# Performance work log

Hardware: AMD Instinct MI355X
Metric: run time of the kernel (lower is better)

Reference implementation:

```python
import jax, jax.numpy as jnp
import numpy as np

HIDDEN_DIM = 1024
SEQ_LEN = 4096
D_IN = 1024


def setup_inputs() -> dict:
    key = jax.random.key(0)
    ks = jax.random.split(key, 9)
    s = 1.0 / np.sqrt(D_IN)
    return {
        "q": jax.random.normal(ks[0], (SEQ_LEN, D_IN), jnp.float32),
        "k": jax.random.normal(ks[1], (SEQ_LEN, D_IN), jnp.float32),
        "v": jax.random.normal(ks[2], (SEQ_LEN, D_IN), jnp.float32),
        "Wq": jax.random.normal(ks[3], (D_IN, HIDDEN_DIM), jnp.float32) * s,
        "bq": jnp.zeros((HIDDEN_DIM,), jnp.float32),
        "Wk": jax.random.normal(ks[4], (D_IN, HIDDEN_DIM), jnp.float32) * s,
        "bk": jnp.zeros((HIDDEN_DIM,), jnp.float32),
        "Wv": jax.random.normal(ks[5], (D_IN, HIDDEN_DIM), jnp.float32) * s,
        "bv": jnpp_zeros() if False else jnp.zeros((HIDDEN_DIM,), jnp.float32),
    }


def reference(q, k, v, Wq, bq, Wk, bk, Wv, bv):
    # Dense projections (flax Dense: x @ W + b)
    query = q @ Wq + bq          # [S, H]
    key_p = k @ Wk + bk          # [S, H]
    value = v @ Wv + bv          # [S, H]
    # scores = Q K^T / sqrt(hidden_dim)  -> [S, S]
    scores = jnp.matmul(query, key_p.T) / jnp.sqrt(jnp.float32(HIDDEN_DIM))
    weights = jax.nn.softmax(scores, axis=-1)
    context = jnp.matmul(weights, value)  # [S, H]
    return context
```

## Files before the change

### kernel.cpp

```cpp
#include <hip/hip_runtime.h>


typedef short short4v __attribute__((ext_vector_type(4)));
typedef short short8  __attribute__((ext_vector_type(8)));
typedef float f32x4   __attribute__((ext_vector_type(4)));

#define MFMA16 __builtin_amdgcn_mfma_f32_16x16x32_bf16

__device__ __forceinline__ short f2bf(float f) {
    union { float f; unsigned u; } x; x.f = f;
    unsigned r = (x.u + 0x7FFFu + ((x.u >> 16) & 1u)) >> 16;
    return (short)r;
}
__device__ __forceinline__ float bf2f(short s) {
    union { unsigned u; float f; } x;
    x.u = ((unsigned)(unsigned short)s) << 16; return x.f;
}
__device__ __forceinline__ void store_out(short* p, float v) { *p = f2bf(v); }
__device__ __forceinline__ void store_out(float* p, float v) { *p = v; }

__device__ __forceinline__ void gl2lds(const short* g, short* l) {
    __builtin_amdgcn_global_load_lds(
        (const __attribute__((address_space(1))) void*)g,
        (__attribute__((address_space(3))) void*)l, 16, 0, 0);
}

__global__ __launch_bounds__(256) void prep_w(
    const float* __restrict__ W0, const float* __restrict__ W1,
    const float* __restrict__ W2, short* __restrict__ Wt)
{
    __shared__ float tile[64][65];
    const float* W = blockIdx.z == 0 ? W0 : (blockIdx.z == 1 ? W1 : W2);
    short* T = Wt + (size_t)blockIdx.z * 1048576;
    const int c0 = blockIdx.x * 64;
    const int r0 = blockIdx.y * 64;
    const int tx = threadIdx.x & 63;
    const int ty = threadIdx.x >> 6;
    #pragma unroll
    for (int p = 0; p < 16; ++p) {
        int r = ty + p * 4;
        tile[r][tx] = W[(size_t)(r0 + r) * 1024 + c0 + tx];
    }
    __syncthreads();
    #pragma unroll
    for (int p = 0; p < 16; ++p) {
        int r = ty + p * 4;
        T[(size_t)(c0 + r) * 1024 + r0 + tx] = f2bf(tile[tx][r]);
    }
}

__global__ __launch_bounds__(256) void cast_qkv(
    const float* __restrict__ q, const float* __restrict__ k,
    const float* __restrict__ v, short* __restrict__ xb)
{
    const float* src = blockIdx.z == 0 ? q : (blockIdx.z == 1 ? k : v);
    short* dst = xb + (size_t)blockIdx.z * 4194304;
    for (int i = blockIdx.x * 256 + threadIdx.x; i < 1048576; i += 256 * 1024) {
        float4 f = ((const float4*)src)[i];
        short4v o;
        o[0] = f2bf(f.x); o[1] = f2bf(f.y); o[2] = f2bf(f.z); o[3] = f2bf(f.w);
        ((short4v*)dst)[i] = o;
    }
}

__global__ __launch_bounds__(256) void transpose_bf16(
    const short* __restrict__ in, short* __restrict__ out, int R, int C)
{
    __shared__ short tile[64][66];
    const int c0 = blockIdx.x * 64;
    const int r0 = blockIdx.y * 64;
    const int tx = threadIdx.x & 63;
    const int ty = threadIdx.x >> 6;
    #pragma unroll
    for (int p = 0; p < 16; ++p) {
        int r = ty + p * 4;
        tile[r][tx] = in[(size_t)(r0 + r) * C + c0 + tx];
    }
    __syncthreads();
    #pragma unroll
    for (int p = 0; p < 16; ++p) {
        int r = ty + p * 4;
        out[(size_t)(c0 + r) * R + r0 + tx] = tile[tx][r];
    }
}

template <typename TOut, int MODE>
__global__ __launch_bounds__(256) void gemm_lds(
    const short* __restrict__ A, const short* __restrict__ Bt,
    const float* __restrict__ b0, const float* __restrict__ b1,
    const float* __restrict__ b2, TOut* __restrict__ C,
    int M, int N, int Kd, int lda, int ldb, float scale, int kiters)
{
    __shared__ short As[128 * 32];
    __shared__ short Bs[128 * 32];

    const int t    = threadIdx.x;
    const int lane = t & 63;
    const int wv   = t >> 6;
    const int n0 = blockIdx.x * 128;
    const int m0 = blockIdx.y * 128;

    const float* bias = nullptr;
    int kbeg = 0;
    if constexpr (MODE == 1) {
        const int z = blockIdx.z;
        A  += (size_t)z * M * lda;
        Bt += (size_t)z * N * ldb;
        C  += (size_t)z * M * N;
        bias = z == 0 ? b0 : (z == 1 ? b1 : b2);
    }
    if constexpr (MODE == 2) {
        kbeg = blockIdx.z * kiters * 32;
        C += (size_t)blockIdx.z * M * N;
    }
    (void)b0; (void)b1; (void)b2;

    const int srow = wv * 32 + (lane >> 2);
    const int cl   = ((lane & 3) ^ ((lane >> 4) & 3)) * 8;
    const short* pA0 = A  + (size_t)(m0 + srow) * lda + kbeg + cl;
    const short* pA1 = pA0 + (size_t)16 * lda;
    const short* pB0 = Bt + (size_t)(n0 + srow) * ldb + kbeg + cl;
    const short* pB1 = pB0 + (size_t)16 * ldb;
    short* lA0 = &As[(wv * 2 + 0) * 512];
    short* lA1 = &As[(wv * 2 + 1) * 512];
    short* lB0 = &Bs[(wv * 2 + 0) * 512];
    short* lB1 = &Bs[(wv * 2 + 1) * 512];

    const int wm = wv & 1, wn = wv >> 1;
    const int lr = lane & 15, lq = lane >> 4;
    const int swz = ((lq ^ ((lr >> 2) & 3))) * 8;

    f32x4 acc[4][4];
    #pragma unroll
    for (int i = 0; i < 4; ++i)
        #pragma unroll
        for (int j = 0; j < 4; ++j) {
            f32x4 z = {0.f, 0.f, 0.f, 0.f};
            acc[i][j] = z;
        }

    for (int kk = 0; kk < kiters; ++kk) {
        gl2lds(pA0, lA0); gl2lds(pA1, lA1);
        gl2lds(pB0, lB0); gl2lds(pB1, lB1);
        pA0 += 32; pA1 += 32; pB0 += 32; pB1 += 32;
        __syncthreads();

        short8 af[4], bfr[4];
        #pragma unroll
        for (int i = 0; i < 4; ++i)
            af[i] = *(const short8*)&As[(wm * 64 + i * 16 + lr) * 32 + swz];
        #pragma unroll
        for (int j = 0; j < 4; ++j)
            bfr[j] = *(const short8*)&Bs[(wn * 64 + j * 16 + lr) * 32 + swz];
        #pragma unroll
        for (int i = 0; i < 4; ++i)
            #pragma unroll
            for (int j = 0; j < 4; ++j)
                acc[i][j] = MFMA16(af[i], bfr[j], acc[i][j], 0, 0, 0);
        __syncthreads();
    }

    #pragma unroll
    for (int i = 0; i < 4; ++i) {
        #pragma unroll
        for (int j = 0; j < 4; ++j) {
            const int crow = m0 + wm * 64 + i * 16 + lq * 4;
            const int ccol = n0 + wn * 64 + j * 16 + lr;
            float bb = 0.f;
            if constexpr (MODE == 1) bb = bias[ccol];
            #pragma unroll
            for (int r = 0; r < 4; ++r) {
                float val = acc[i][j][r] * scale + bb;
                store_out(&C[(size_t)(crow + r) * N + ccol], val);
            }
        }
    }
}

__global__ __launch_bounds__(256) void softmax_bf16(short* __restrict__ S)
{
    const int row = blockIdx.x;
    short8* r8 = (short8*)(S + (size_t)row * 4096);
    const int t = threadIdx.x;

    float x[16];
    #pragma unroll
    for (int i = 0; i < 2; ++i) {
        short8 raw = r8[t + 256 * i];
        #pragma unroll
        for (int j = 0; j < 8; ++j) x[8 * i + j] = bf2f(raw[j]);
    }
    float m = -1e30f;
    #pragma unroll
    for (int i = 0; i < 16; ++i) m = fmaxf(m, x[i]);
    #pragma unroll
    for (int off = 32; off > 0; off >>= 1) m = fmaxf(m, __shfl_xor(m, off));

    __shared__ float redm[4], reds[4];
    const int wv = t >> 6;
    if ((t & 63) == 0) redm[wv] = m;
    __syncthreads();
    m = fmaxf(fmaxf(redm[0], redm[1]), fmaxf(redm[2], redm[3]));

    float s = 0.f;
    #pragma unroll
    for (int i = 0; i < 16; ++i) { x[i] = __expf(x[i] - m); s += x[i]; }
    #pragma unroll
    for (int off = 32; off > 0; off >>= 1) s += __shfl_xor(s, off);
    if ((t & 63) == 0) reds[wv] = s;
    __syncthreads();
    s = reds[0] + reds[1] + reds[2] + reds[3];
    const float inv = 1.f / s;

    #pragma unroll
    for (int i = 0; i < 2; ++i) {
        short8 o;
        #pragma unroll
        for (int j = 0; j < 8; ++j) o[j] = f2bf(x[8 * i + j] * inv);
        r8[t + 256 * i] = o;
    }
}

__global__ __launch_bounds__(256) void combine(
    const float* __restrict__ p0, const float* __restrict__ p1,
    float* __restrict__ out)
{
    for (int i = blockIdx.x * 256 + threadIdx.x; i < 1048576; i += 256 * 1024) {
        float4 a = ((const float4*)p0)[i];
        float4 b = ((const float4*)p1)[i];
        float4 o; o.x = a.x + b.x; o.y = a.y + b.y;
        o.z = a.z + b.z; o.w = a.w + b.w;
        ((float4*)out)[i] = o;
    }
}

extern "C" void kernel_launch(void* const* d_in, const int* in_sizes, int n_in,
                              void* d_out, int out_size, void* d_ws, size_t ws_size,
                              hipStream_t stream)
{
    const float* q  = (const float*)d_in[0];
    const float* k  = (const float*)d_in[1];
    const float* v  = (const float*)d_in[2];
    const float* Wq = (const float*)d_in[3];
    const float* bq = (const float*)d_in[4];
    const float* Wk = (const float*)d_in[5];
    const float* bk = (const float*)d_in[6];
    const float* Wv = (const float*)d_in[7];
    const float* bv = (const float*)d_in[8];
    float* out = (float*)d_out;

    char* ws = (char*)d_ws;
    const size_t MB = 1ull << 20;
    short* Wt = (short*)(ws + 0);
    short* xb = (short*)(ws + 6 * MB);
    short* pr = (short*)(ws + 30 * MB);
    short* Vt = (short*)(ws + 54 * MB);
    short* S  = (short*)(ws + 62 * MB);
    float* p0 = (float*)(ws + 0);
    float* p1 = p0 + 4194304;

    prep_w<<<dim3(16, 16, 3), 256, 0, stream>>>(Wq, Wk, Wv, Wt);
    cast_qkv<<<dim3(1024, 1, 3), 256, 0, stream>>>(q, k, v, xb);
    gemm_lds<short, 1><<<dim3(8, 32, 3), 256, 0, stream>>>(
        xb, Wt, bq, bk, bv, pr, 4096, 1024, 1024, 1024, 1024, 1.f, 32);
    transpose_bf16<<<dim3(16, 64), 256, 0, stream>>>(pr + 2 * 4194304, Vt, 4096, 1024);
    gemm_lds<short, 0><<<dim3(32, 32), 256, 0, stream>>>(
        pr, pr + 4194304, nullptr, nullptr, nullptr, S,
        4096, 4096, 1024, 1024, 1024, 0.03125f, 32);
    softmax_bf16<<<4096, 256, 0, stream>>>(S);
    gemm_lds<float, 2><<<dim3(8, 32, 2), 256, 0, stream>>>(
        S, Vt, nullptr, nullptr, nullptr, p0,
        4096, 1024, 4096, 4096, 4096, 1.f, 64);
    combine<<<1024, 256, 0, stream>>>(p0, p1, out);
}
```

Measured before the change: 293.3 us.

## Deepen GEMM K-tile to 64, add grouped rasterization, fuse V transpose into projection

The GEMM kernel now stages 64-wide K slices with an XOR swizzle, which halves the number of loop iterations and barriers. Blocks are remapped into groups of 8 row-tiles to improve L2 reuse. The V projection blocks write a transposed output through LDS, so the separate transpose kernel is removed and Vt reuses the freed workspace region. The cost is doubled LDS per block, which may reduce occupancy.

```diff
diff --git a/kernel.cpp b/kernel.cpp
--- a/kernel.cpp
+++ b/kernel.cpp
@@ -63,42 +63,29 @@
     }
 }
 
-__global__ __launch_bounds__(256) void transpose_bf16(
-    const short* __restrict__ in, short* __restrict__ out, int R, int C)
-{
-    __shared__ short tile[64][66];
-    const int c0 = blockIdx.x * 64;
-    const int r0 = blockIdx.y * 64;
-    const int tx = threadIdx.x & 63;
-    const int ty = threadIdx.x >> 6;
-    #pragma unroll
-    for (int p = 0; p < 16; ++p) {
-        int r = ty + p * 4;
-        tile[r][tx] = in[(size_t)(r0 + r) * C + c0 + tx];
-    }
-    __syncthreads();
-    #pragma unroll
-    for (int p = 0; p < 16; ++p) {
-        int r = ty + p * 4;
-        out[(size_t)(c0 + r) * R + r0 + tx] = tile[tx][r];
-    }
-}
-
 template <typename TOut, int MODE>
-__global__ __launch_bounds__(256) void gemm_lds(
+__global__ __launch_bounds__(256) void gemm64(
     const short* __restrict__ A, const short* __restrict__ Bt,
     const float* __restrict__ b0, const float* __restrict__ b1,
     const float* __restrict__ b2, TOut* __restrict__ C,
+    short* __restrict__ Vt,
     int M, int N, int Kd, int lda, int ldb, float scale, int kiters)
 {
-    __shared__ short As[128 * 32];
-    __shared__ short Bs[128 * 32];
+    constexpr int LDSN = (MODE == 1) ? (128 * 136) : (128 * 64 * 2);
+    __shared__ short Lds[LDSN];
+    short* As = Lds;
+    short* Bs = Lds + 128 * 64;
 
     const int t    = threadIdx.x;
     const int lane = t & 63;
     const int wv   = t >> 6;
-    const int n0 = blockIdx.x * 128;
-    const int m0 = blockIdx.y * 128;
+
+    const int nb  = gridDim.x;
+    const int bid = blockIdx.y * nb + blockIdx.x;
+    const int band   = bid / (8 * nb);
+    const int within = bid - band * 8 * nb;
+    const int m0 = (band * 8 + (within & 7)) * 128;
+    const int n0 = (within >> 3) * 128;
 
     const float* bias = nullptr;
     int kbeg = 0;
@@ -110,25 +97,23 @@
         bias = z == 0 ? b0 : (z == 1 ? b1 : b2);
     }
     if constexpr (MODE == 2) {
-        kbeg = blockIdx.z * kiters * 32;
+        kbeg = blockIdx.z * kiters * 64;
         C += (size_t)blockIdx.z * M * N;
     }
     (void)b0; (void)b1; (void)b2;
 
-    const int srow = wv * 32 + (lane >> 2);
-    const int cl   = ((lane & 3) ^ ((lane >> 4) & 3)) * 8;
-    const short* pA0 = A  + (size_t)(m0 + srow) * lda + kbeg + cl;
-    const short* pA1 = pA0 + (size_t)16 * lda;
-    const short* pB0 = Bt + (size_t)(n0 + srow) * ldb + kbeg + cl;
-    const short* pB1 = pB0 + (size_t)16 * ldb;
-    short* lA0 = &As[(wv * 2 + 0) * 512];
-    short* lA1 = &As[(wv * 2 + 1) * 512];
-    short* lB0 = &Bs[(wv * 2 + 0) * 512];
-    short* lB1 = &Bs[(wv * 2 + 1) * 512];
+    const int sr = lane >> 3;
+    const int sc = (lane & 7) ^ sr;
+    const short* pA = A  + (size_t)(m0 + wv * 32 + sr) * lda + kbeg + sc * 8;
+    const short* pB = Bt + (size_t)(n0 + wv * 32 + sr) * ldb + kbeg + sc * 8;
+    const size_t a8 = (size_t)8 * lda;
+    const size_t b8 = (size_t)8 * ldb;
+    short* lA = As + wv * 2048;
+    short* lB = Bs + wv * 2048;
 
     const int wm = wv & 1, wn = wv >> 1;
     const int lr = lane & 15, lq = lane >> 4;
-    const int swz = ((lq ^ ((lr >> 2) & 3))) * 8;
+    const int xkey = lr & 7;
 
     f32x4 acc[4][4];
     #pragma unroll
@@ -140,26 +125,58 @@
         }
 
     for (int kk = 0; kk < kiters; ++kk) {
-        gl2lds(pA0, lA0); gl2lds(pA1, lA1);
-        gl2lds(pB0, lB0); gl2lds(pB1, lB1);
-        pA0 += 32; pA1 += 32; pB0 += 32; pB1 += 32;
+        #pragma unroll
+        for (int r = 0; r < 4; ++r) gl2lds(pA + r * a8, lA + r * 512);
+        #pragma unroll
+        for (int r = 0; r < 4; ++r) gl2lds(pB + r * b8, lB + r * 512);
+        pA += 64; pB += 64;
         __syncthreads();
 
-        short8 af[4], bfr[4];
-        #pragma unroll
-        for (int i = 0; i < 4; ++i)
-            af[i] = *(const short8*)&As[(wm * 64 + i * 16 + lr) * 32 + swz];
-        #pragma unroll
-        for (int j = 0; j < 4; ++j)
-            bfr[j] = *(const short8*)&Bs[(wn * 64 + j * 16 + lr) * 32 + swz];
-        #pragma unroll
-        for (int i = 0; i < 4; ++i)
+        #pragma unroll
+        for (int h = 0; h < 2; ++h) {
+            short8 af[4], bfr[4];
+            #pragma unroll
+            for (int i = 0; i < 4; ++i)
+                af[i] = *(const short8*)
+                    &As[(wm * 64 + i * 16 + lr) * 64 + (((h * 4 + lq) ^ xkey) * 8)];
             #pragma unroll
             for (int j = 0; j < 4; ++j)
-                acc[i][j] = MFMA16(af[i], bfr[j], acc[i][j], 0, 0, 0);
+                bfr[j] = *(const short8*)
+                    &Bs[(wn * 64 + j * 16 + lr) * 64 + (((h * 4 + lq) ^ xkey) * 8)];
+            #pragma unroll
+            for (int i = 0; i < 4; ++i)
+                #pragma unroll
+                for (int j = 0; j < 4; ++j)
+                    acc[i][j] = MFMA16(af[i], bfr[j], acc[i][j], 0, 0, 0);
+        }
         __syncthreads();
     }
 
+    if constexpr (MODE == 1) {
+        if (blockIdx.z == 2) {
+            #pragma unroll
+            for (int i = 0; i < 4; ++i) {
+                #pragma unroll
+                for (int j = 0; j < 4; ++j) {
+                    const int colL = wn * 64 + j * 16 + lr;
+                    const float bb = bias[n0 + colL];
+                    #pragma unroll
+                    for (int r = 0; r < 4; ++r) {
+                        const int rowL = wm * 64 + i * 16 + lq * 4 + r;
+                        Lds[colL * 136 + rowL] = f2bf(acc[i][j][r] * scale + bb);
+                    }
+                }
+            }
+            __syncthreads();
+            const int c = t >> 1, part = t & 1;
+            short* dst = Vt + (size_t)(n0 + c) * 4096 + m0 + part * 64;
+            #pragma unroll
+            for (int s = 0; s < 8; ++s)
+                *(short8*)(dst + s * 8) =
+                    *(const short8*)&Lds[c * 136 + part * 64 + s * 8];
+            return;
+        }
+    }
     #pragma unroll
     for (int i = 0; i < 4; ++i) {
         #pragma unroll
@@ -254,22 +271,21 @@
     short* Wt = (short*)(ws + 0);
     short* xb = (short*)(ws + 6 * MB);
     short* pr = (short*)(ws + 30 * MB);
-    short* Vt = (short*)(ws + 54 * MB);
-    short* S  = (short*)(ws + 62 * MB);
+    short* Vt = (short*)(ws + 46 * MB);
+    short* S  = (short*)(ws + 54 * MB);
     float* p0 = (float*)(ws + 0);
     float* p1 = p0 + 4194304;
 
     prep_w<<<dim3(16, 16, 3), 256, 0, stream>>>(Wq, Wk, Wv, Wt);
     cast_qkv<<<dim3(1024, 1, 3), 256, 0, stream>>>(q, k, v, xb);
-    gemm_lds<short, 1><<<dim3(8, 32, 3), 256, 0, stream>>>(
-        xb, Wt, bq, bk, bv, pr, 4096, 1024, 1024, 1024, 1024, 1.f, 32);
-    transpose_bf16<<<dim3(16, 64), 256, 0, stream>>>(pr + 2 * 4194304, Vt, 4096, 1024);
-    gemm_lds<short, 0><<<dim3(32, 32), 256, 0, stream>>>(
-        pr, pr + 4194304, nullptr, nullptr, nullptr, S,
-        4096, 4096, 1024, 1024, 1024, 0.03125f, 32);
+    gemm64<short, 1><<<dim3(8, 32, 3), 256, 0, stream>>>(
+        xb, Wt, bq, bk, bv, pr, Vt, 4096, 1024, 1024, 1024, 1024, 1.f, 16);
+    gemm64<short, 0><<<dim3(32, 32), 256, 0, stream>>>(
+        pr, pr + 4194304, nullptr, nullptr, nullptr, S, nullptr,
+        4096, 4096, 1024, 1024, 1024, 0.03125f, 16);
     softmax_bf16<<<4096, 256, 0, stream>>>(S);
-    gemm_lds<float, 2><<<dim3(8, 32, 2), 256, 0, stream>>>(
-        S, Vt, nullptr, nullptr, nullptr, p0,
-        4096, 1024, 4096, 4096, 4096, 1.f, 64);
+    gemm64<float, 2><<<dim3(8, 32, 2), 256, 0, stream>>>(
+        S, Vt, nullptr, nullptr, nullptr, p0, nullptr,
+        4096, 1024, 4096, 4096, 4096, 1.f, 32);
     combine<<<1024, 256, 0, stream>>>(p0, p1, out);
 }
```

Result: faster. 268.0 us (-8.6%).
